# Performance work log

Hardware: AMD Instinct MI355X
Metric: run time of the kernel (lower is better)

The kernel has to match this reference:

```python
import jax, jax.numpy as jnp
import numpy as np

B, S, H, NH = 2, 2048, 1024, 16
HD = H // NH
BASE = 10000.0


def _rotate_half(x):
    x1, x2 = x[..., : x.shape[-1] // 2], x[..., x.shape[-1] // 2 :]
    return jnp.concatenate((-x2, x1), axis=-1)


def setup_inputs() -> dict:
    key = jax.random.key(0)
    ks = jax.random.split(key, 6)
    hidden_states = jax.random.normal(ks[0], (B, S, H), jnp.float32)
    scale = 0.02
    wq = jax.random.normal(ks[1], (H, H), jnp.float32) * scale
    wk = jax.random.normal(ks[2], (H, H), jnp.float32) * scale
    wv = jax.random.normal(ks[3], (H, H), jnp.float32) * scale
    wo = jax.random.normal(ks[4], (H, H), jnp.float32) * scale
    # additive causal mask, shape (B, 1, S, S): 0 on/below diagonal, large negative above
    neg = jnp.finfo(jnp.float32).min
    causal = jnp.where(jnp.tril(jnp.ones((S, S), dtype=bool)), 0.0, neg).astype(jnp.float32)
    attention_mask = jnp.broadcast_to(causal[None, None], (B, 1, S, S))
    position_ids = jnp.broadcast_to(jnp.arange(S, dtype=jnp.int32)[None], (B, S))
    return {
        "hidden_states": hidden_states,
        "attention_mask": attention_mask,
        "wq": wq,
        "wk": wk,
        "wv": wv,
        "wo": wo,
        "position_ids": position_ids,
    }


def reference(hidden_states, attention_mask, wq, wk, wv, wo, position_ids):
    b, s, h = hidden_states.shape
    dtype = hidden_states.dtype

    def proj(x, w):  # torch Linear: y = x @ w.T, then split heads -> (b, nh, s, hd)
        y = jnp.einsum("bsh,oh->bso", x, w)
        return y.reshape(b, s, NH, HD).transpose(0, 2, 1, 3)

    q = proj(hidden_states, wq)
    k = proj(hidden_states, wk)
    v = proj(hidden_states, wv)

    # rotary cache (computed in fp32 like torch), gathered by position_ids
    inv_freq = 1.0 / (BASE ** (jnp.arange(0, HD, 2, dtype=jnp.float32) / HD))
    t = jnp.arange(s, dtype=jnp.float32)
    freqs = jnp.outer(t, inv_freq)                  # (s, hd/2)
    emb = jnp.concatenate((freqs, freqs), axis=-1)  # (s, hd)
    pos = jnp.clip(position_ids, 0, s - 1)
    cos = jnp.cos(emb).astype(dtype)[pos][:, None]  # (b, 1, s, hd)
    sin = jnp.sin(emb).astype(dtype)[pos][:, None]

    q = q * cos + _rotate_half(q) * sin
    k = k * cos + _rotate_half(k) * sin

    scores = jnp.einsum("bhqd,bhkd->bhqk", q, k) / jnp.sqrt(jnp.asarray(HD, dtype))
    scores = scores + attention_mask
    attn = jax.nn.softmax(scores.astype(jnp.float32), axis=-1).astype(dtype)
    out = jnp.einsum("bhqk,bhkd->bhqd", attn, v)    # (b, nh, s, hd)
    out = out.transpose(0, 2, 1, 3).reshape(b, s, h)
    return jnp.einsum("bso,ho->bsh", out, wo)
```

## Files before the change

kernel.cpp:

```cpp
#include <hip/hip_runtime.h>
#include <cstdint>
#include <cstddef>

typedef unsigned short u16;
typedef __bf16 bf16x8 __attribute__((ext_vector_type(8)));
typedef float f32x4 __attribute__((ext_vector_type(4)));

constexpr int SEQ = 2048;
constexpr int HID = 1024;
constexpr int NHEAD = 16;
constexpr int HDIM = 64;

typedef __attribute__((address_space(1))) void gvoid;
typedef __attribute__((address_space(3))) void lvoid;

__device__ __forceinline__ u16 f2bf(float f) {
  union { float f; unsigned u; } v;
  v.f = f;
  unsigned r = v.u + 0x7fffu + ((v.u >> 16) & 1u);
  return (u16)(r >> 16);
}
__device__ __forceinline__ u16 f2bf_trunc(float f) {
  union { float f; unsigned u; } v;
  v.f = f;
  return (u16)(v.u >> 16);
}

__device__ __forceinline__ f32x4 mfma16(bf16x8 a, bf16x8 b, f32x4 c) {
  return __builtin_amdgcn_mfma_f32_16x16x32_bf16(a, b, c, 0, 0, 0);
}

__device__ __forceinline__ int detect_f32(const unsigned* __restrict__ hs) {
  unsigned w = hs[threadIdx.x & 63];
  u16 lo = (u16)(w & 0xffffu);
  int e = (lo >> 7) & 0xff;
  bool inr = (e >= 100 && e <= 154);
  unsigned long long m = __ballot(inr);
  return (__popcll(m) >= 48) ? 0 : 1;
}

__global__ __launch_bounds__(256) void cvt_kernel(
    const void* s0, const void* s1, const void* s2, const void* s3, const void* s4,
    u16* __restrict__ d0, u16* __restrict__ dW,
    float* __restrict__ cosb, float* __restrict__ sinb) {
  int b = blockIdx.x;
  if (b >= 4096) {
    int idx = (b - 4096) * 256 + threadIdx.x;
    int s = idx >> 5;
    int i = idx & 31;
    float inv_freq = expf(-(float)(2 * i) * (9.210340371976184f / 64.0f));
    float ang = (float)s * inv_freq;
    float c = cosf(ang), sn = sinf(ang);
    cosb[s * 64 + i]      = c;
    cosb[s * 64 + i + 32] = c;
    sinb[s * 64 + i]      = sn;
    sinb[s * 64 + i + 32] = sn;
    return;
  }
  const int is_f32 = detect_f32((const unsigned*)s0);
  const void* s; u16* d; long base;
  if (b < 2048) { s = s0; d = d0; base = (long)b * 2048; }
  else {
    int bb = b - 2048;
    int w = bb >> 9;
    base = (long)(bb & 511) * 2048;
    s = (w == 0) ? s1 : (w == 1) ? s2 : (w == 2) ? s3 : s4;
    d = dW + (long)w * 1048576;
  }
  long idx = base + (long)threadIdx.x * 8;
  if (is_f32) {
    const float* sf = (const float*)s;
    float4 a = *(const float4*)(sf + idx);
    float4 c = *(const float4*)(sf + idx + 4);
    ushort4 p0, p1;
    p0.x = f2bf(a.x); p0.y = f2bf(a.y); p0.z = f2bf(a.z); p0.w = f2bf(a.w);
    p1.x = f2bf(c.x); p1.y = f2bf(c.y); p1.z = f2bf(c.z); p1.w = f2bf(c.w);
    *(ushort4*)(d + idx) = p0;
    *(ushort4*)(d + idx + 4) = p1;
  } else {
    const u16* su = (const u16*)s;
    *(uint4*)(d + idx) = *(const uint4*)(su + idx);
  }
}

__device__ __forceinline__ void gemm_mainloop_128(
    const u16* __restrict__ Ag, const u16* __restrict__ Bg,
    int row0, int col0, f32x4 acc[4][4]) {
  __shared__ __align__(16) u16 As[2][128 * 64];
  __shared__ __align__(16) u16 Bs[2][128 * 64];
  const int t = threadIdx.x;
  const int lane = t & 63, wave = t >> 6;
  const int l15 = lane & 15, quad = lane >> 4;
  const int wm = wave >> 1, wn = wave & 1;
  const int cs = ((lane & 7) ^ ((lane >> 3) & 7)) * 8;
  const u16* aS = Ag + (size_t)(row0 + wave * 32 + (lane >> 3)) * 1024 + cs;
  const u16* bS = Bg + (size_t)(col0 + wave * 32 + (lane >> 3)) * 1024 + cs;
  const int swz0 = ((quad)     ^ (l15 & 7)) * 8;
  const int swz1 = ((4 + quad) ^ (l15 & 7)) * 8;

#define STAGE_AB(bi, k0_) do {                                                   \
    _Pragma("unroll")                                                            \
    for (int j = 0; j < 4; j++) {                                                \
      __builtin_amdgcn_global_load_lds((gvoid*)(aS + (k0_) + j * 8192),          \
          (lvoid*)(&As[bi][0] + wave * 2048 + j * 512), 16, 0, 0);               \
      __builtin_amdgcn_global_load_lds((gvoid*)(bS + (k0_) + j * 8192),          \
          (lvoid*)(&Bs[bi][0] + wave * 2048 + j * 512), 16, 0, 0);               \
    }                                                                            \
  } while (0)

  STAGE_AB(0, 0);
  int cur = 0;
  for (int k0 = 0; k0 < 1024; k0 += 64) {
    if (k0 + 64 < 1024) {
      STAGE_AB(cur ^ 1, k0 + 64);
      asm volatile("s_waitcnt vmcnt(8)" ::: "memory");
    } else {
      asm volatile("s_waitcnt vmcnt(0)" ::: "memory");
    }
    __builtin_amdgcn_sched_barrier(0);
    __builtin_amdgcn_s_barrier();
    __builtin_amdgcn_sched_barrier(0);
    const u16* Asb = &As[cur][0];
    const u16* Bsb = &Bs[cur][0];
#pragma unroll
    for (int kk = 0; kk < 2; kk++) {
      const int sw = kk ? swz1 : swz0;
      bf16x8 af[4], bfr[4];
#pragma unroll
      for (int i = 0; i < 4; i++)
        af[i] = *(const bf16x8*)(Asb + (wm * 64 + i * 16 + l15) * 64 + sw);
#pragma unroll
      for (int j = 0; j < 4; j++)
        bfr[j] = *(const bf16x8*)(Bsb + (wn * 64 + j * 16 + l15) * 64 + sw);
#pragma unroll
      for (int i = 0; i < 4; i++)
#pragma unroll
        for (int j = 0; j < 4; j++)
          acc[i][j] = mfma16(af[i], bfr[j], acc[i][j]);
    }
    __builtin_amdgcn_sched_barrier(0);
    __builtin_amdgcn_s_barrier();
    __builtin_amdgcn_sched_barrier(0);
    cur ^= 1;
  }
#undef STAGE_AB
}

__global__ __launch_bounds__(256) void qkv_kernel(
    const u16* __restrict__ X, const u16* __restrict__ Wcat,
    const int* __restrict__ pos_ids,
    const float* __restrict__ cosb, const float* __restrict__ sinb,
    u16* __restrict__ q_ws, u16* __restrict__ k_ws, u16* __restrict__ vt_ws) {
  const int row0 = blockIdx.x * 128;
  const int col0 = blockIdx.y * 128;
  const int z = col0 >> 10;
  f32x4 acc[4][4];
#pragma unroll
  for (int i = 0; i < 4; i++)
#pragma unroll
    for (int j = 0; j < 4; j++) acc[i][j] = f32x4{0.f, 0.f, 0.f, 0.f};

  gemm_mainloop_128(X, Wcat, row0, col0, acc);

  const int t = threadIdx.x;
  const int lane = t & 63, wave = t >> 6;
  const int l15 = lane & 15, quad = lane >> 4;
  const int wm = wave >> 1, wn = wave & 1;
  const int gr0 = row0 + wm * 64;
  const int gc0 = col0 + wn * 64;
  const int nh = (gc0 >> 6) & 15;
  const float qscale = (z == 0) ? 0.18033688011112042f : 1.0f;

  if (z < 2) {
    u16* dst = (z == 0) ? q_ws : k_ws;
#pragma unroll
    for (int i = 0; i < 4; i++) {
#pragma unroll
      for (int r = 0; r < 4; r++) {
        int m = gr0 + i * 16 + quad * 4 + r;
        int b = m >> 11, s = m & 2047;
        int p = pos_ids[m];
        p = min(max(p, 0), SEQ - 1);
#pragma unroll
        for (int j = 0; j < 4; j++) {
          int d = j * 16 + l15;
          float c = cosb[p * 64 + d];
          float sn = sinb[p * 64 + d];
          float v = acc[i][j][r];
          float partner = acc[i][j ^ 2][r];
          float rot = (j < 2) ? -partner : partner;
          float o = (v * c + rot * sn) * qscale;
          dst[((size_t)((b * NHEAD + nh) * SEQ + s) << 6) + d] = f2bf(o);
        }
      }
    }
  } else {
#pragma unroll
    for (int i = 0; i < 4; i++) {
      int m_base = gr0 + i * 16 + quad * 4;
      int b = m_base >> 11, s = m_base & 2047;
#pragma unroll
      for (int j = 0; j < 4; j++) {
        int d = j * 16 + l15;
        ushort4 pk;
        pk.x = f2bf(acc[i][j][0]);
        pk.y = f2bf(acc[i][j][1]);
        pk.z = f2bf(acc[i][j][2]);
        pk.w = f2bf(acc[i][j][3]);
        *(ushort4*)(vt_ws + ((size_t)((b * NHEAD + nh) * 64 + d)) * SEQ + s) = pk;
      }
    }
  }
}

__global__ __launch_bounds__(256) void attn_kernel(
    const u16* __restrict__ q_ws, const u16* __restrict__ k_ws,
    const u16* __restrict__ vt_ws, u16* __restrict__ attn_ws) {
  const int b = blockIdx.z;
  const int qt = b ? blockIdx.x : 15 - blockIdx.x;
  const int nh = blockIdx.y;
  const int bh = b * NHEAD + nh;
  __shared__ __align__(16) u16 Ks[2][128 * 64];
  __shared__ __align__(16) u16 Vts[2][64 * 128];
  __shared__ __align__(16) u16 Pl[128 * 64];

  const int t = threadIdx.x;
  const int lane = t & 63, wave = t >> 6;
  const int l15 = lane & 15, quad = lane >> 4;
  const int l7 = l15 & 7;
  const int wq0 = qt * 128 + wave * 32;

  bf16x8 aq[2][2];
#pragma unroll
  for (int i = 0; i < 2; i++) {
    const u16* qb = q_ws + ((size_t)bh * SEQ + wq0 + i * 16 + l15) * 64;
    aq[i][0] = *(const bf16x8*)(qb + quad * 8);
    aq[i][1] = *(const bf16x8*)(qb + 32 + quad * 8);
  }

  f32x4 O[2][4];
  float lp[2];
#pragma unroll
  for (int i = 0; i < 2; i++) {
    lp[i] = 0.f;
#pragma unroll
    for (int n = 0; n < 4; n++) O[i][n] = f32x4{0.f, 0.f, 0.f, 0.f};
  }

  const int krl = lane >> 3;
  const int kcs = ((lane & 7) ^ (krl & 7)) * 8;
  const u16* kS = k_ws + (size_t)bh * SEQ * 64 + (size_t)(wave * 32 + krl) * 64 + kcs;
  const int vrl = lane >> 4;
  const int vc4 = lane & 15;
  const u16* vS = vt_ws + (size_t)bh * 64 * SEQ + (size_t)(wave * 16 + vrl) * SEQ;
  int vx[4];
#pragma unroll
  for (int j = 0; j < 4; j++) vx[j] = (vc4 ^ ((4 * j + vrl) & 15)) * 8;

#define STAGE_KV(bi, kt_) do {                                                     \
    const size_t koff_ = (size_t)(kt_) * 8192;                                     \
    _Pragma("unroll")                                                              \
    for (int j = 0; j < 4; j++) {                                                  \
      __builtin_amdgcn_global_load_lds((gvoid*)(kS + koff_ + j * 512),             \
          (lvoid*)(&Ks[bi][0] + wave * 2048 + j * 512), 16, 0, 0);                 \
      __builtin_amdgcn_global_load_lds(                                            \
          (gvoid*)(vS + (size_t)j * 4 * SEQ + (kt_) * 128 + vx[j]),                \
          (lvoid*)(&Vts[bi][0] + wave * 2048 + j * 512), 16, 0, 0);                \
    }                                                                              \
  } while (0)

  const int nkt = qt + 1;
  STAGE_KV(0, 0);
  int cur = 0;
  for (int kt = 0; kt < nkt; ++kt) {
    if (kt + 1 < nkt) {
      STAGE_KV(cur ^ 1, kt + 1);
      asm volatile("s_waitcnt vmcnt(8)" ::: "memory");
    } else {
      asm volatile("s_waitcnt vmcnt(0)" ::: "memory");
    }
    __builtin_amdgcn_sched_barrier(0);
    __builtin_amdgcn_s_barrier();
    __builtin_amdgcn_sched_barrier(0);
    const u16* Ksb = &Ks[cur][0];
    const u16* Vtb = &Vts[cur][0];

#pragma unroll
    for (int h = 0; h < 2; h++) {
      f32x4 sc[2][4];
      __builtin_amdgcn_s_setprio(1);
#pragma unroll
      for (int ct = 0; ct < 4; ct++) {
        const u16* krow = Ksb + (h * 64 + ct * 16 + l15) * 64;
        bf16x8 bk0 = *(const bf16x8*)(krow + (quad ^ l7) * 8);
        bf16x8 bk1 = *(const bf16x8*)(krow + ((4 + quad) ^ l7) * 8);
#pragma unroll
        for (int i = 0; i < 2; i++) {
          f32x4 z = f32x4{0.f, 0.f, 0.f, 0.f};
          z = mfma16(bk0, aq[i][0], z);
          z = mfma16(bk1, aq[i][1], z);
          sc[i][ct] = z;
        }
      }
      __builtin_amdgcn_s_setprio(0);

      const int kbase = kt * 128 + h * 64;
      if (kt == qt) {
#pragma unroll
        for (int i = 0; i < 2; i++) {
          const int qrow = wq0 + i * 16 + l15;
          const int prow = (wave * 32 + i * 16 + l15) * 64;
#pragma unroll
          for (int ct = 0; ct < 4; ct++) {
            const int key0 = kbase + ct * 16 + quad * 4;
            float p[4];
#pragma unroll
            for (int r = 0; r < 4; r++) {
              float e = __builtin_amdgcn_exp2f(sc[i][ct][r]);
              if (key0 + r > qrow) e = 0.f;
              p[r] = e;
            }
            lp[i] += (p[0] + p[1]) + (p[2] + p[3]);
            ushort4 pk;
            pk.x = f2bf_trunc(p[0]); pk.y = f2bf_trunc(p[1]);
            pk.z = f2bf_trunc(p[2]); pk.w = f2bf_trunc(p[3]);
            *(ushort4*)&Pl[prow + ((ct * 2 + (quad >> 1)) ^ l7) * 8 + (quad & 1) * 4] = pk;
          }
        }
      } else {
#pragma unroll
        for (int i = 0; i < 2; i++) {
          const int prow = (wave * 32 + i * 16 + l15) * 64;
#pragma unroll
          for (int ct = 0; ct < 4; ct++) {
            float p[4];
#pragma unroll
            for (int r = 0; r < 4; r++) p[r] = __builtin_amdgcn_exp2f(sc[i][ct][r]);
            lp[i] += (p[0] + p[1]) + (p[2] + p[3]);
            ushort4 pk;
            pk.x = f2bf_trunc(p[0]); pk.y = f2bf_trunc(p[1]);
            pk.z = f2bf_trunc(p[2]); pk.w = f2bf_trunc(p[3]);
            *(ushort4*)&Pl[prow + ((ct * 2 + (quad >> 1)) ^ l7) * 8 + (quad & 1) * 4] = pk;
          }
        }
      }

      bf16x8 pa[2][2];
#pragma unroll
      for (int i = 0; i < 2; i++) {
        const u16* prow = Pl + (wave * 32 + i * 16 + l15) * 64;
        pa[i][0] = *(const bf16x8*)(prow + (quad ^ l7) * 8);
        pa[i][1] = *(const bf16x8*)(prow + ((4 + quad) ^ l7) * 8);
      }
      __builtin_amdgcn_s_setprio(1);
#pragma unroll
      for (int n = 0; n < 4; n++) {
        const u16* vrow = Vtb + (n * 16 + l15) * 128;
        bf16x8 bv0 = *(const bf16x8*)(vrow + ((h * 8 + quad) ^ l15) * 8);
        bf16x8 bv1 = *(const bf16x8*)(vrow + ((h * 8 + 4 + quad) ^ l15) * 8);
#pragma unroll
        for (int i = 0; i < 2; i++) {
          O[i][n] = mfma16(pa[i][0], bv0, O[i][n]);
          O[i][n] = mfma16(pa[i][1], bv1, O[i][n]);
        }
      }
      __builtin_amdgcn_s_setprio(0);
    }

    __builtin_amdgcn_sched_barrier(0);
    __builtin_amdgcn_s_barrier();
    __builtin_amdgcn_sched_barrier(0);
    cur ^= 1;
  }
#undef STAGE_KV

#pragma unroll
  for (int i = 0; i < 2; i++) {
    float l = lp[i];
    l += __shfl_xor(l, 16, 64);
    l += __shfl_xor(l, 32, 64);
#pragma unroll
    for (int r = 0; r < 4; r++) {
      float inv = 1.0f / __shfl(l, quad * 4 + r, 64);
      int q = wq0 + i * 16 + quad * 4 + r;
      size_t base = ((size_t)(b * SEQ + q)) * HID + nh * 64;
#pragma unroll
      for (int n = 0; n < 4; n++)
        attn_ws[base + n * 16 + l15] = f2bf(O[i][n][r] * inv);
    }
  }
}

__global__ __launch_bounds__(256) void out_proj_kernel(
    const u16* __restrict__ A, const u16* __restrict__ Wo, void* __restrict__ out,
    const unsigned* __restrict__ hs_raw) {
  __shared__ __align__(16) u16 As[2][64 * 64];
  __shared__ __align__(16) u16 Bs[2][128 * 64];
  const int row0 = blockIdx.x * 64;
  const int col0 = blockIdx.y * 128;
  const int is_f32 = detect_f32(hs_raw);
  const int t = threadIdx.x;
  const int lane = t & 63, wave = t >> 6;
  const int l15 = lane & 15, quad = lane >> 4;
  const int wm = wave >> 1, wn = wave & 1;
  const int cs = ((lane & 7) ^ ((lane >> 3) & 7)) * 8;
  const u16* aS = A  + (size_t)(row0 + wave * 16 + (lane >> 3)) * 1024 + cs;
  const u16* bS = Wo + (size_t)(col0 + wave * 32 + (lane >> 3)) * 1024 + cs;
  const int swz0 = ((quad)     ^ (l15 & 7)) * 8;
  const int swz1 = ((4 + quad) ^ (l15 & 7)) * 8;

  f32x4 acc[2][4];
#pragma unroll
  for (int i = 0; i < 2; i++)
#pragma unroll
    for (int j = 0; j < 4; j++) acc[i][j] = f32x4{0.f, 0.f, 0.f, 0.f};

#define STAGE_OP(bi, k0_) do {                                                   \
    _Pragma("unroll")                                                            \
    for (int j = 0; j < 2; j++)                                                  \
      __builtin_amdgcn_global_load_lds((gvoid*)(aS + (k0_) + j * 8192),          \
          (lvoid*)(&As[bi][0] + wave * 1024 + j * 512), 16, 0, 0);               \
    _Pragma("unroll")                                                            \
    for (int j = 0; j < 4; j++)                                                  \
      __builtin_amdgcn_global_load_lds((gvoid*)(bS + (k0_) + j * 8192),          \
          (lvoid*)(&Bs[bi][0] + wave * 2048 + j * 512), 16, 0, 0);               \
  } while (0)

  STAGE_OP(0, 0);
  int cur = 0;
  for (int k0 = 0; k0 < 1024; k0 += 64) {
    if (k0 + 64 < 1024) {
      STAGE_OP(cur ^ 1, k0 + 64);
      asm volatile("s_waitcnt vmcnt(6)" ::: "memory");
    } else {
      asm volatile("s_waitcnt vmcnt(0)" ::: "memory");
    }
    __builtin_amdgcn_sched_barrier(0);
    __builtin_amdgcn_s_barrier();
    __builtin_amdgcn_sched_barrier(0);
    const u16* Asb = &As[cur][0];
    const u16* Bsb = &Bs[cur][0];
#pragma unroll
    for (int kk = 0; kk < 2; kk++) {
      const int sw = kk ? swz1 : swz0;
      bf16x8 af[2], bfr[4];
#pragma unroll
      for (int i = 0; i < 2; i++)
        af[i] = *(const bf16x8*)(Asb + (wm * 32 + i * 16 + l15) * 64 + sw);
#pragma unroll
      for (int j = 0; j < 4; j++)
        bfr[j] = *(const bf16x8*)(Bsb + (wn * 64 + j * 16 + l15) * 64 + sw);
#pragma unroll
      for (int i = 0; i < 2; i++)
#pragma unroll
        for (int j = 0; j < 4; j++)
          acc[i][j] = mfma16(af[i], bfr[j], acc[i][j]);
    }
    __builtin_amdgcn_sched_barrier(0);
    __builtin_amdgcn_s_barrier();
    __builtin_amdgcn_sched_barrier(0);
    cur ^= 1;
  }
#undef STAGE_OP

  const int gr0 = row0 + wm * 32;
  const int gc0 = col0 + wn * 64;
#pragma unroll
  for (int i = 0; i < 2; i++)
#pragma unroll
    for (int r = 0; r < 4; r++) {
      int m = gr0 + i * 16 + quad * 4 + r;
      if (is_f32) {
        float* o = (float*)out;
#pragma unroll
        for (int j = 0; j < 4; j++)
          o[(size_t)m * 1024 + gc0 + j * 16 + l15] = acc[i][j][r];
      } else {
        u16* o = (u16*)out;
#pragma unroll
        for (int j = 0; j < 4; j++)
          o[(size_t)m * 1024 + gc0 + j * 16 + l15] = f2bf(acc[i][j][r]);
      }
    }
}

extern "C" void kernel_launch(void* const* d_in, const int* in_sizes, int n_in,
                              void* d_out, int out_size, void* d_ws, size_t ws_size,
                              hipStream_t stream) {
  const void* hs = d_in[0];
  const void* wq = d_in[2];
  const void* wk = d_in[3];
  const void* wv = d_in[4];
  const void* wo = d_in[5];
  const int* pos = (const int*)d_in[6];

  char* ws = (char*)d_ws;
  float* cosb = (float*)ws;
  float* sinb = (float*)(ws + (512 << 10));
  u16* xbf    = (u16*)(ws + (1 << 20));
  u16* wcat   = xbf + (size_t)4194304;
  u16* q_ws   = wcat + (size_t)4 * 1048576;
  u16* k_ws   = q_ws + (size_t)2 * NHEAD * SEQ * HDIM;
  u16* vt_ws  = k_ws + (size_t)2 * NHEAD * SEQ * HDIM;
  u16* attn_ws = vt_ws + (size_t)2 * NHEAD * SEQ * HDIM;

  cvt_kernel<<<4352, 256, 0, stream>>>(hs, wq, wk, wv, wo, xbf, wcat, cosb, sinb);
  qkv_kernel<<<dim3(32, 24), 256, 0, stream>>>(xbf, wcat, pos, cosb, sinb,
                                               q_ws, k_ws, vt_ws);
  attn_kernel<<<dim3(16, NHEAD, 2), 256, 0, stream>>>(q_ws, k_ws, vt_ws, attn_ws);
  out_proj_kernel<<<dim3(64, 8), 256, 0, stream>>>(attn_ws, wcat + (size_t)3 * 1048576,
                                                   d_out, (const unsigned*)hs);
}
```

Measured before the change: 197.8 us.

## Use 256x256 tiles with 8 waves and phased MFMA/LDS pipeline in QKV GEMM

```diff
diff --git a/kernel.cpp b/kernel.cpp
--- a/kernel.cpp
+++ b/kernel.cpp
@@ -83,98 +83,136 @@
   }
 }
 
-__device__ __forceinline__ void gemm_mainloop_128(
+__device__ __forceinline__ void gemm_mainloop_256(
     const u16* __restrict__ Ag, const u16* __restrict__ Bg,
-    int row0, int col0, f32x4 acc[4][4]) {
-  __shared__ __align__(16) u16 As[2][128 * 64];
-  __shared__ __align__(16) u16 Bs[2][128 * 64];
+    int row0, int col0, f32x4 acc[8][4]) {
+  __shared__ __align__(16) u16 As[2][256 * 64];
+  __shared__ __align__(16) u16 Bs[2][256 * 64];
   const int t = threadIdx.x;
   const int lane = t & 63, wave = t >> 6;
   const int l15 = lane & 15, quad = lane >> 4;
-  const int wm = wave >> 1, wn = wave & 1;
-  const int cs = ((lane & 7) ^ ((lane >> 3) & 7)) * 8;
-  const u16* aS = Ag + (size_t)(row0 + wave * 32 + (lane >> 3)) * 1024 + cs;
-  const u16* bS = Bg + (size_t)(col0 + wave * 32 + (lane >> 3)) * 1024 + cs;
+  const int wm = wave >> 2, wn = wave & 3;
+  const int srow = lane >> 3;
+  const int cs = ((lane & 7) ^ srow) * 8;
+  const u16* aS = Ag + (size_t)(row0 + wave * 32 + srow) * 1024 + cs;
+  const u16* bS = Bg + (size_t)(col0 + wave * 32 + srow) * 1024 + cs;
   const int swz0 = ((quad)     ^ (l15 & 7)) * 8;
   const int swz1 = ((4 + quad) ^ (l15 & 7)) * 8;
 
-#define STAGE_AB(bi, k0_) do {                                                   \
-    _Pragma("unroll")                                                            \
-    for (int j = 0; j < 4; j++) {                                                \
+#define STAGE_A(bi, k0_) do {                                                    \
+    _Pragma("unroll")                                                            \
+    for (int j = 0; j < 4; j++)                                                  \
       __builtin_amdgcn_global_load_lds((gvoid*)(aS + (k0_) + j * 8192),          \
           (lvoid*)(&As[bi][0] + wave * 2048 + j * 512), 16, 0, 0);               \
+  } while (0)
+#define STAGE_B(bi, k0_) do {                                                    \
+    _Pragma("unroll")                                                            \
+    for (int j = 0; j < 4; j++)                                                  \
       __builtin_amdgcn_global_load_lds((gvoid*)(bS + (k0_) + j * 8192),          \
           (lvoid*)(&Bs[bi][0] + wave * 2048 + j * 512), 16, 0, 0);               \
+  } while (0)
+#define PBAR() do {                                                              \
+    __builtin_amdgcn_sched_barrier(0);                                           \
+    __builtin_amdgcn_s_barrier();                                                \
+    __builtin_amdgcn_sched_barrier(0);                                           \
+  } while (0)
+#define READ_AF(QM) do {                                                         \
+    _Pragma("unroll")                                                            \
+    for (int mi = 0; mi < 4; mi++) {                                             \
+      const u16* ap = Ab + (wm * 128 + (QM) * 64 + mi * 16 + l15) * 64;          \
+      af[mi][0] = *(const bf16x8*)(ap + swz0);                                   \
+      af[mi][1] = *(const bf16x8*)(ap + swz1);                                   \
     }                                                                            \
   } while (0)
-
-  STAGE_AB(0, 0);
-  int cur = 0;
-  for (int k0 = 0; k0 < 1024; k0 += 64) {
-    if (k0 + 64 < 1024) {
-      STAGE_AB(cur ^ 1, k0 + 64);
-      asm volatile("s_waitcnt vmcnt(8)" ::: "memory");
-    } else {
-      asm volatile("s_waitcnt vmcnt(0)" ::: "memory");
-    }
-    __builtin_amdgcn_sched_barrier(0);
-    __builtin_amdgcn_s_barrier();
-    __builtin_amdgcn_sched_barrier(0);
-    const u16* Asb = &As[cur][0];
-    const u16* Bsb = &Bs[cur][0];
-#pragma unroll
-    for (int kk = 0; kk < 2; kk++) {
-      const int sw = kk ? swz1 : swz0;
-      bf16x8 af[4], bfr[4];
-#pragma unroll
-      for (int i = 0; i < 4; i++)
-        af[i] = *(const bf16x8*)(Asb + (wm * 64 + i * 16 + l15) * 64 + sw);
-#pragma unroll
-      for (int j = 0; j < 4; j++)
-        bfr[j] = *(const bf16x8*)(Bsb + (wn * 64 + j * 16 + l15) * 64 + sw);
-#pragma unroll
-      for (int i = 0; i < 4; i++)
-#pragma unroll
-        for (int j = 0; j < 4; j++)
-          acc[i][j] = mfma16(af[i], bfr[j], acc[i][j]);
-    }
-    __builtin_amdgcn_sched_barrier(0);
-    __builtin_amdgcn_s_barrier();
-    __builtin_amdgcn_sched_barrier(0);
-    cur ^= 1;
-  }
-#undef STAGE_AB
-}
-
-__global__ __launch_bounds__(256) void qkv_kernel(
+#define READ_BF(NB) do {                                                         \
+    _Pragma("unroll")                                                            \
+    for (int nj = 0; nj < 2; nj++) {                                             \
+      const u16* bp = Bb + (wn * 64 + ((NB) + nj) * 16 + l15) * 64;              \
+      bfr[nj][0] = *(const bf16x8*)(bp + swz0);                                  \
+      bfr[nj][1] = *(const bf16x8*)(bp + swz1);                                  \
+    }                                                                            \
+  } while (0)
+#define MFMA_PH(QM, NB) do {                                                     \
+    __builtin_amdgcn_s_setprio(1);                                               \
+    _Pragma("unroll")                                                            \
+    for (int mi = 0; mi < 4; mi++)                                               \
+    _Pragma("unroll")                                                            \
+    for (int nj = 0; nj < 2; nj++)                                               \
+    _Pragma("unroll")                                                            \
+    for (int kk = 0; kk < 2; kk++)                                               \
+      acc[(QM) * 4 + mi][(NB) + nj] =                                            \
+          mfma16(af[mi][kk], bfr[nj][kk], acc[(QM) * 4 + mi][(NB) + nj]);        \
+    __builtin_amdgcn_s_setprio(0);                                               \
+  } while (0)
+
+  STAGE_A(0, 0);
+  STAGE_B(0, 0);
+  asm volatile("s_waitcnt vmcnt(0)" ::: "memory");
+  PBAR();
+
+  for (int kt = 0; kt < 16; ++kt) {
+    const int cur = kt & 1;
+    const u16* Ab = &As[cur][0];
+    const u16* Bb = &Bs[cur][0];
+    const bool pf = (kt + 1 < 16);
+    bf16x8 af[4][2], bfr[2][2];
+    READ_AF(0); READ_BF(0);
+    if (pf) STAGE_A(cur ^ 1, (kt + 1) * 64);
+    PBAR();
+    MFMA_PH(0, 0);
+    PBAR();
+    READ_BF(2);
+    if (pf) STAGE_B(cur ^ 1, (kt + 1) * 64);
+    PBAR();
+    MFMA_PH(0, 2);
+    PBAR();
+    READ_AF(1); READ_BF(0);
+    PBAR();
+    MFMA_PH(1, 0);
+    PBAR();
+    READ_BF(2);
+    PBAR();
+    MFMA_PH(1, 2);
+    if (pf) asm volatile("s_waitcnt vmcnt(0)" ::: "memory");
+    PBAR();
+  }
+#undef STAGE_A
+#undef STAGE_B
+#undef PBAR
+#undef READ_AF
+#undef READ_BF
+#undef MFMA_PH
+}
+
+__global__ __launch_bounds__(512, 2) void qkv_kernel(
     const u16* __restrict__ X, const u16* __restrict__ Wcat,
     const int* __restrict__ pos_ids,
     const float* __restrict__ cosb, const float* __restrict__ sinb,
     u16* __restrict__ q_ws, u16* __restrict__ k_ws, u16* __restrict__ vt_ws) {
-  const int row0 = blockIdx.x * 128;
-  const int col0 = blockIdx.y * 128;
-  const int z = col0 >> 10;
-  f32x4 acc[4][4];
-#pragma unroll
-  for (int i = 0; i < 4; i++)
+  const int row0 = blockIdx.x * 256;
+  const int col0 = blockIdx.y * 256;
+  f32x4 acc[8][4];
+#pragma unroll
+  for (int i = 0; i < 8; i++)
 #pragma unroll
     for (int j = 0; j < 4; j++) acc[i][j] = f32x4{0.f, 0.f, 0.f, 0.f};
 
-  gemm_mainloop_128(X, Wcat, row0, col0, acc);
+  gemm_mainloop_256(X, Wcat, row0, col0, acc);
 
   const int t = threadIdx.x;
   const int lane = t & 63, wave = t >> 6;
   const int l15 = lane & 15, quad = lane >> 4;
-  const int wm = wave >> 1, wn = wave & 1;
-  const int gr0 = row0 + wm * 64;
+  const int wm = wave >> 2, wn = wave & 3;
+  const int gr0 = row0 + wm * 128;
   const int gc0 = col0 + wn * 64;
+  const int z = gc0 >> 10;
   const int nh = (gc0 >> 6) & 15;
   const float qscale = (z == 0) ? 0.18033688011112042f : 1.0f;
 
   if (z < 2) {
     u16* dst = (z == 0) ? q_ws : k_ws;
 #pragma unroll
-    for (int i = 0; i < 4; i++) {
+    for (int i = 0; i < 8; i++) {
 #pragma unroll
       for (int r = 0; r < 4; r++) {
         int m = gr0 + i * 16 + quad * 4 + r;
@@ -196,7 +234,7 @@
     }
   } else {
 #pragma unroll
-    for (int i = 0; i < 4; i++) {
+    for (int i = 0; i < 8; i++) {
       int m_base = gr0 + i * 16 + quad * 4;
       int b = m_base >> 11, s = m_base & 2047;
 #pragma unroll
@@ -505,7 +543,7 @@
   u16* attn_ws = vt_ws + (size_t)2 * NHEAD * SEQ * HDIM;
 
   cvt_kernel<<<4352, 256, 0, stream>>>(hs, wq, wk, wv, wo, xbf, wcat, cosb, sinb);
-  qkv_kernel<<<dim3(32, 24), 256, 0, stream>>>(xbf, wcat, pos, cosb, sinb,
+  qkv_kernel<<<dim3(16, 12), 512, 0, stream>>>(xbf, wcat, pos, cosb, sinb,
                                                q_ws, k_ws, vt_ws);
   attn_kernel<<<dim3(16, NHEAD, 2), 256, 0, stream>>>(q_ws, k_ws, vt_ws, attn_ws);
   out_proj_kernel<<<dim3(64, 8), 256, 0, stream>>>(attn_ws, wcat + (size_t)3 * 1048576,
```

Result: no change. 195.4 us (-1.2%).
